# Performance work log

Measured on AMD Instinct MI355X. Metric: run time of the kernel, lower is better.

Reference implementation:

```python
import jax, jax.numpy as jnp
import numpy as np

N = 1024      # number of nodes
D = 128       # d_x
H = 8         # num_heads


def setup_inputs() -> dict:
    key = jax.random.key(0)
    ks = jax.random.split(key, 7)
    s = (D * H) ** -0.5
    return {
        "x": jax.random.normal(ks[0], (N, D), dtype=jnp.float32),
        "spatial_encoding": jax.random.normal(ks[1], (N, N), dtype=jnp.float32),
        "edge_encoding": jax.random.normal(ks[2], (N, N), dtype=jnp.float32),
        "Wq": jax.random.normal(ks[3], (D * H, D), dtype=jnp.float32) * s,
        "Wk": jax.random.normal(ks[4], (D * H, D), dtype=jnp.float32) * s,
        "Wv": jax.random.normal(ks[5], (D * H, D), dtype=jnp.float32) * s,
        "Wo": jax.random.normal(ks[6], (D, D * H), dtype=jnp.float32) * s,
    }


def reference(x, spatial_encoding, edge_encoding, Wq, Wk, Wv, Wo):
    n, d = x.shape
    h = Wq.shape[0] // d
    scale = d ** -0.5
    # Linear (no bias), then the module's peculiar view: [n, d*h] -> [d, n, h]
    q = (x @ Wq.T).reshape(d, n, h)            # [d, n, h]
    k = (x @ Wk.T).reshape(d, n, h)            # [d, n, h]
    v = (x @ Wv.T).reshape(d, n, h)            # [d, n, h]
    # a = q @ k^T over head dim: [d, n, n]
    a = jnp.einsum('dnh,dmh->dnm', q, k) * scale
    a = a + spatial_encoding + edge_encoding   # [n,n] biases broadcast over d
    a = jax.nn.softmax(a, axis=2)
    # dropout is identity at inference
    out = jnp.einsum('dnm,dmh->dnh', a, v)     # [d, n, h]
    out = out.reshape(n, h * d)                # row-major reshape, same as torch
    return out @ Wo.T                          # [n, d]
```

## Files before the change

kernel.cpp:

```cpp
#include <hip/hip_runtime.h>
#include <hip/hip_bf16.h>
#include <math.h>

#define N_NODES 1024
#define D_DIM   128
#define H_HEADS 8
#define DH      1024

typedef short  short8 __attribute__((ext_vector_type(8)));
typedef float  f32x16 __attribute__((ext_vector_type(16)));
typedef float  f32x4  __attribute__((ext_vector_type(4)));
typedef unsigned short us4 __attribute__((ext_vector_type(4)));

static __device__ __forceinline__ unsigned short f2bf(float x) {
    __hip_bfloat16 h = __float2bfloat16(x);
    return *reinterpret_cast<unsigned short*>(&h);
}
static __device__ __forceinline__ unsigned cvt_pk_bf16(float lo, float hi) {
    unsigned r;
    asm volatile("v_cvt_pk_bf16_f32 %0, %1, %2" : "=v"(r) : "v"(lo), "v"(hi));
    return r;
}
static __device__ __forceinline__ void permlane32_swap(unsigned &a, unsigned &b) {
    asm volatile("v_permlane32_swap_b32 %0, %1" : "+v"(a), "+v"(b));
}
static __device__ __forceinline__ float fast_exp2(float x) {
    float r;
    asm("v_exp_f32 %0, %1" : "=v"(r) : "v"(x));
    return r;
}

__global__ __launch_bounds__(256) void prep_kernel(const float* __restrict__ x,
                                                   const float* __restrict__ Wq,
                                                   const float* __restrict__ Wk,
                                                   const float* __restrict__ Wv,
                                                   const float* __restrict__ sp,
                                                   const float* __restrict__ ed,
                                                   unsigned short* __restrict__ Q,
                                                   unsigned short* __restrict__ K,
                                                   unsigned short* __restrict__ V,
                                                   float* __restrict__ Bq) {
    __shared__ float tile[32][33];
    const int bid = blockIdx.x;
    const int tid = threadIdx.x;

    if (bid < 768) {
        const int lane = tid & 63, wvi = tid >> 6;
        const int l31 = lane & 31, hi = lane >> 5;
        const int m   = bid >> 8;
        const int rem = bid & 255;
        const int rb0 = (rem & 7) * 128 + wvi * 32;
        const int col = (rem >> 3) * 32 + l31;
        const float* W        = (m == 0) ? Wq : (m == 1) ? Wk : Wv;
        unsigned short* Out   = (m == 0) ? Q  : (m == 1) ? K  : V;
        const float osc = (m == 0) ? 0.12751879523173864f : 1.0f;

        const float* xrow = x + (size_t)(rb0 + l31) * 128 + 8 * hi;
        const float* wrow = W + (size_t)col * 128 + 8 * hi;

        f32x16 acc = {};
        #pragma unroll
        for (int ks = 0; ks < 8; ++ks) {
            float4 xa = *reinterpret_cast<const float4*>(xrow + ks * 16);
            float4 xb = *reinterpret_cast<const float4*>(xrow + ks * 16 + 4);
            float4 wa = *reinterpret_cast<const float4*>(wrow + ks * 16);
            float4 wb = *reinterpret_cast<const float4*>(wrow + ks * 16 + 4);
            union { short8 s8; unsigned u[4]; } af, bf;
            af.u[0] = cvt_pk_bf16(xa.x, xa.y); af.u[1] = cvt_pk_bf16(xa.z, xa.w);
            af.u[2] = cvt_pk_bf16(xb.x, xb.y); af.u[3] = cvt_pk_bf16(xb.z, xb.w);
            bf.u[0] = cvt_pk_bf16(wa.x, wa.y); bf.u[1] = cvt_pk_bf16(wa.z, wa.w);
            bf.u[2] = cvt_pk_bf16(wb.x, wb.y); bf.u[3] = cvt_pk_bf16(wb.z, wb.w);
            acc = __builtin_amdgcn_mfma_f32_32x32x16_bf16(af.s8, bf.s8, acc, 0, 0, 0);
        }
        #pragma unroll
        for (int i = 0; i < 16; ++i) {
            int mm = (i & 3) + 8 * (i >> 2) + 4 * hi;
            Out[(size_t)(rb0 + mm) * DH + col] = f2bf(acc[i] * osc);
        }
    } else {
        const int b2 = bid - 768;
        const int cb = b2 & 31, rb = b2 >> 5;
        const float L2E = 1.4426950408889634f;
        for (int i = tid; i < 1024; i += 256) {
            int rr = i >> 5, cc = i & 31;
            size_t g = (size_t)(rb * 32 + rr) * 1024 + cb * 32 + cc;
            tile[rr][cc] = (sp[g] + ed[g]) * L2E;
        }
        __syncthreads();
        const int c4l = tid >> 5, rr = tid & 31;
        float4 v = make_float4(tile[rr][4 * c4l + 0], tile[rr][4 * c4l + 1],
                               tile[rr][4 * c4l + 2], tile[rr][4 * c4l + 3]);
        reinterpret_cast<float4*>(Bq)[(size_t)(cb * 8 + c4l) * 1024 + rb * 32 + rr] = v;
    }
}

__global__ __launch_bounds__(256) void attn_kernel(const unsigned short* __restrict__ Qb,
                                                   const unsigned short* __restrict__ Kb,
                                                   const unsigned short* __restrict__ Vb,
                                                   const float* __restrict__ Bq,
                                                   float* __restrict__ Opart,
                                                   float* __restrict__ Lpart) {
    __shared__ unsigned short Vt[9 * 512];
    const int dd = blockIdx.y, ch = blockIdx.z;
    const int tid = threadIdx.x, lane = tid & 63, wvi = tid >> 6;
    const int l31 = lane & 31, hi = lane >> 5;

    {
        const unsigned short* src = Vb + (size_t)dd * 8192 + (size_t)ch * 4096;
        char* base = reinterpret_cast<char*>(Vt);
        int pr = tid;
        short8 v0 = *reinterpret_cast<const short8*>(src + (size_t)(2 * pr) * 8);
        short8 v1 = *reinterpret_cast<const short8*>(src + (size_t)(2 * pr + 1) * 8);
        #pragma unroll
        for (int h = 0; h < 8; ++h) {
            unsigned d = (unsigned)(unsigned short)v0[h] |
                         ((unsigned)(unsigned short)v1[h] << 16);
            *reinterpret_cast<unsigned*>(base + h * 1024 + ((4 * pr) ^ (h << 4))) = d;
        }
        reinterpret_cast<unsigned*>(base + 8 * 1024)[tid] = 0x3F803F80u;
    }
    __syncthreads();

    const int r = blockIdx.x * 128 + wvi * 32 + l31;
    short8 qf = {};
    if (!hi) qf = *reinterpret_cast<const short8*>(Qb + (size_t)dd * 8192 + (size_t)r * 8);

    f32x16 oacc = {};
    const unsigned short* kp = Kb + (size_t)dd * 8192 + (size_t)(ch * 512 + l31) * 8;
    const float4* bq4 = reinterpret_cast<const float4*>(Bq)
                        + (size_t)ch * 131072 + (size_t)hi * 1024 + r;

    auto load_bias = [&](int cbv) -> f32x16 {
        const float4* b = bq4 + (size_t)cbv * 8192;
        float4 b0 = b[0], b1 = b[2048], b2 = b[4096], b3 = b[6144];
        f32x16 o;
        o[0] = b0.x; o[1] = b0.y; o[2]  = b0.z; o[3]  = b0.w;
        o[4] = b1.x; o[5] = b1.y; o[6]  = b1.z; o[7]  = b1.w;
        o[8] = b2.x; o[9] = b2.y; o[10] = b2.z; o[11] = b2.w;
        o[12] = b3.x; o[13] = b3.y; o[14] = b3.z; o[15] = b3.w;
        return o;
    };
    auto load_k = [&](int cbv) -> short8 {
        return *reinterpret_cast<const short8*>(kp + (size_t)cbv * 256);
    };
    auto step = [&](int cbv, const f32x16& bias, const short8& kfv) {
        f32x16 sf = bias;
        sf = __builtin_amdgcn_mfma_f32_32x32x16_bf16(kfv, qf, sf, 0, 0, 0);
        float p[16];
        #pragma unroll
        for (int i = 0; i < 16; ++i) p[i] = fast_exp2(sf[i]);
        unsigned u0 = cvt_pk_bf16(p[0],  p[1]);
        unsigned u1 = cvt_pk_bf16(p[2],  p[3]);
        unsigned u2 = cvt_pk_bf16(p[4],  p[5]);
        unsigned u3 = cvt_pk_bf16(p[6],  p[7]);
        unsigned u4 = cvt_pk_bf16(p[8],  p[9]);
        unsigned u5 = cvt_pk_bf16(p[10], p[11]);
        unsigned u6 = cvt_pk_bf16(p[12], p[13]);
        unsigned u7 = cvt_pk_bf16(p[14], p[15]);
        permlane32_swap(u0, u2);
        permlane32_swap(u1, u3);
        permlane32_swap(u4, u6);
        permlane32_swap(u5, u7);
        union { short8 s8; unsigned u[4]; } pb1, pb2;
        pb1.u[0] = u0; pb1.u[1] = u1; pb1.u[2] = u2; pb1.u[3] = u3;
        pb2.u[0] = u4; pb2.u[1] = u5; pb2.u[2] = u6; pb2.u[3] = u7;

        short8 vf1 = {}, vf2 = {};
        if (l31 < 9) {
            const char* vb = reinterpret_cast<const char*>(Vt) + l31 * 1024;
            vf1 = *reinterpret_cast<const short8*>(vb + ((cbv * 64 + 16 * hi)      ^ (l31 << 4)));
            vf2 = *reinterpret_cast<const short8*>(vb + ((cbv * 64 + 32 + 16 * hi) ^ (l31 << 4)));
        }
        oacc = __builtin_amdgcn_mfma_f32_32x32x16_bf16(vf1, pb1.s8, oacc, 0, 0, 0);
        oacc = __builtin_amdgcn_mfma_f32_32x32x16_bf16(vf2, pb2.s8, oacc, 0, 0, 0);
    };

    f32x16 bA = load_bias(0), bB = load_bias(1);
    short8 kA = load_k(0),   kB = load_k(1);
    for (int cb = 0; cb < 16; cb += 2) {
        step(cb, bA, kA);
        if (cb < 14) { bA = load_bias(cb + 2); kA = load_k(cb + 2); }
        step(cb + 1, bB, kB);
        if (cb < 14) { bB = load_bias(cb + 3); kB = load_k(cb + 3); }
    }

    size_t off = (size_t)ch * 1048576 + (size_t)dd * 8192 + (size_t)r * 8 + 4 * hi;
    *reinterpret_cast<float4*>(Opart + off) =
        make_float4(oacc[0], oacc[1], oacc[2], oacc[3]);
    if (!hi) Lpart[(size_t)ch * 131072 + (size_t)dd * 1024 + r] = oacc[4];
}

__global__ __launch_bounds__(256) void combine_kernel(const float* __restrict__ Opart,
                                                      const float* __restrict__ Lpart,
                                                      unsigned short* __restrict__ Oh,
                                                      unsigned short* __restrict__ Ol) {
    const int gid = blockIdx.x * 256 + threadIdx.x;
    const float4* p1 = reinterpret_cast<const float4*>(Opart) + (size_t)gid * 2;
    const float4* p2 = reinterpret_cast<const float4*>(Opart + 1048576) + (size_t)gid * 2;
    float4 a0 = p1[0], a1 = p1[1], b0 = p2[0], b1 = p2[1];
    const float rl = 1.f / (Lpart[gid] + Lpart[131072 + gid]);
    float v[8] = { (a0.x + b0.x) * rl, (a0.y + b0.y) * rl,
                   (a0.z + b0.z) * rl, (a0.w + b0.w) * rl,
                   (a1.x + b1.x) * rl, (a1.y + b1.y) * rl,
                   (a1.z + b1.z) * rl, (a1.w + b1.w) * rl };
    union { short8 s8; unsigned short us[8]; } h8, l8;
    #pragma unroll
    for (int i = 0; i < 8; ++i) {
        unsigned uv = __float_as_uint(v[i]);
        h8.us[i] = (unsigned short)(uv >> 16);
        l8.us[i] = f2bf(v[i] - __uint_as_float(uv & 0xFFFF0000u));
    }
    *reinterpret_cast<short8*>(Oh + (size_t)gid * 8) = h8.s8;
    *reinterpret_cast<short8*>(Ol + (size_t)gid * 8) = l8.s8;
}

__global__ __launch_bounds__(256) void oproj_kernel(const unsigned short* __restrict__ Oh,
                                                    const unsigned short* __restrict__ Ol,
                                                    const float* __restrict__ Wo,
                                                    float* __restrict__ out) {
    __shared__ float red[4][256];
    const int tid = threadIdx.x, lane = tid & 63, wvi = tid >> 6;
    const int l15 = lane & 15, kg = lane >> 4;
    const int rbase = blockIdx.x * 16, cbase = blockIdx.y * 16;

    const unsigned short* ah_p = Oh + (size_t)(rbase + l15) * 1024 + wvi * 256 + kg * 8;
    const unsigned short* al_p = Ol + (size_t)(rbase + l15) * 1024 + wvi * 256 + kg * 8;
    const float*          b_p  = Wo + (size_t)(cbase + l15) * 1024 + wvi * 256 + kg * 8;

    f32x4 acc = {};
    #pragma unroll
    for (int ks = 0; ks < 8; ++ks) {
        short8 ah = *reinterpret_cast<const short8*>(ah_p + ks * 32);
        short8 al = *reinterpret_cast<const short8*>(al_p + ks * 32);
        float4 w0 = *reinterpret_cast<const float4*>(b_p + ks * 32);
        float4 w1 = *reinterpret_cast<const float4*>(b_p + ks * 32 + 4);
        float w[8] = { w0.x, w0.y, w0.z, w0.w, w1.x, w1.y, w1.z, w1.w };
        union { short8 s8; unsigned u[4]; } bh, bl;
        #pragma unroll
        for (int j = 0; j < 4; ++j) {
            unsigned e = __float_as_uint(w[2 * j]) >> 16;
            unsigned o = __float_as_uint(w[2 * j + 1]) & 0xFFFF0000u;
            bh.u[j] = e | o;
            float lo0 = w[2 * j]     - __uint_as_float(__float_as_uint(w[2 * j])     & 0xFFFF0000u);
            float lo1 = w[2 * j + 1] - __uint_as_float(__float_as_uint(w[2 * j + 1]) & 0xFFFF0000u);
            bl.u[j] = cvt_pk_bf16(lo0, lo1);
        }
        acc = __builtin_amdgcn_mfma_f32_16x16x32_bf16(ah, bh.s8, acc, 0, 0, 0);
        acc = __builtin_amdgcn_mfma_f32_16x16x32_bf16(al, bh.s8, acc, 0, 0, 0);
        acc = __builtin_amdgcn_mfma_f32_16x16x32_bf16(ah, bl.s8, acc, 0, 0, 0);
    }
    #pragma unroll
    for (int i = 0; i < 4; ++i)
        red[wvi][(kg * 4 + i) * 16 + l15] = acc[i];
    __syncthreads();
    float v = red[0][tid & 255] + red[1][tid & 255] + red[2][tid & 255] + red[3][tid & 255];
    out[(size_t)(rbase + (tid >> 4)) * D_DIM + cbase + (tid & 15)] = v;
}

extern "C" void kernel_launch(void* const* d_in, const int* in_sizes, int n_in,
                              void* d_out, int out_size, void* d_ws, size_t ws_size,
                              hipStream_t stream) {
    const float* x  = (const float*)d_in[0];
    const float* sp = (const float*)d_in[1];
    const float* ed = (const float*)d_in[2];
    const float* Wq = (const float*)d_in[3];
    const float* Wk = (const float*)d_in[4];
    const float* Wv = (const float*)d_in[5];
    const float* Wo = (const float*)d_in[6];
    float* out = (float*)d_out;

    float* ws = (float*)d_ws;
    const size_t M = (size_t)N_NODES * DH;
    float* Bq = ws;
    unsigned short* Qb = (unsigned short*)(ws + M);
    unsigned short* Kb = Qb + M;
    unsigned short* Vb = Kb + M;
    unsigned short* Oh = Vb + M;
    unsigned short* Ol = Oh + M;
    float* Opart = (float*)(Ol + M);
    float* Lpart = Opart + 2 * M;

    prep_kernel<<<dim3(1792), 256, 0, stream>>>(x, Wq, Wk, Wv, sp, ed, Qb, Kb, Vb, Bq);
    attn_kernel<<<dim3(8, 128, 2), 256, 0, stream>>>(Qb, Kb, Vb, Bq, Opart, Lpart);
    combine_kernel<<<dim3(512), 256, 0, stream>>>(Opart, Lpart, Oh, Ol);
    oproj_kernel<<<dim3(64, 8), 256, 0, stream>>>(Oh, Ol, Wo, out);
}
```

Baseline: 66.42 us.

## Process two d-slices per attention block to reuse bias loads; pre-split Wo in prep

Each attention block now handles two d-slices, so the loaded bias tile (the dominant memory stream) is reused across both, and the grid shrinks by half in the y dimension. The V row index is clamped instead of predicated, which removes a branch. Separately, the bf16 hi/lo split of Wo moves into extra prep blocks written to workspace, so oproj loads pre-split bf16 instead of converting fp32 on the fly. The cost is higher register pressure (two accumulators, extra K and Q fragments) and fewer blocks in the attention launch.

```diff
diff --git a/kernel.cpp b/kernel.cpp
--- a/kernel.cpp
+++ b/kernel.cpp
@@ -10,7 +10,6 @@
 typedef short  short8 __attribute__((ext_vector_type(8)));
 typedef float  f32x16 __attribute__((ext_vector_type(16)));
 typedef float  f32x4  __attribute__((ext_vector_type(4)));
-typedef unsigned short us4 __attribute__((ext_vector_type(4)));
 
 static __device__ __forceinline__ unsigned short f2bf(float x) {
     __hip_bfloat16 h = __float2bfloat16(x);
@@ -36,10 +35,13 @@
                                                    const float* __restrict__ Wv,
                                                    const float* __restrict__ sp,
                                                    const float* __restrict__ ed,
+                                                   const float* __restrict__ Wo,
                                                    unsigned short* __restrict__ Q,
                                                    unsigned short* __restrict__ K,
                                                    unsigned short* __restrict__ V,
-                                                   float* __restrict__ Bq) {
+                                                   float* __restrict__ Bq,
+                                                   unsigned short* __restrict__ Woh,
+                                                   unsigned short* __restrict__ Wol) {
     __shared__ float tile[32][33];
     const int bid = blockIdx.x;
     const int tid = threadIdx.x;
@@ -77,7 +79,7 @@
             int mm = (i & 3) + 8 * (i >> 2) + 4 * hi;
             Out[(size_t)(rb0 + mm) * DH + col] = f2bf(acc[i] * osc);
         }
-    } else {
+    } else if (bid < 1792) {
         const int b2 = bid - 768;
         const int cb = b2 & 31, rb = b2 >> 5;
         const float L2E = 1.4426950408889634f;
@@ -91,6 +93,23 @@
         float4 v = make_float4(tile[rr][4 * c4l + 0], tile[rr][4 * c4l + 1],
                                tile[rr][4 * c4l + 2], tile[rr][4 * c4l + 3]);
         reinterpret_cast<float4*>(Bq)[(size_t)(cb * 8 + c4l) * 1024 + rb * 32 + rr] = v;
+    } else {
+        const int b2 = bid - 1792;
+        const size_t base = (size_t)b2 * 4096 + (size_t)tid * 16;
+        #pragma unroll
+        for (int t = 0; t < 4; ++t) {
+            float4 w = *reinterpret_cast<const float4*>(Wo + base + t * 4);
+            float ww[4] = { w.x, w.y, w.z, w.w };
+            unsigned short h4[4], l4[4];
+            #pragma unroll
+            for (int j = 0; j < 4; ++j) {
+                unsigned uv = __float_as_uint(ww[j]);
+                h4[j] = (unsigned short)(uv >> 16);
+                l4[j] = f2bf(ww[j] - __uint_as_float(uv & 0xFFFF0000u));
+            }
+            *reinterpret_cast<uint2*>(Woh + base + t * 4) = *reinterpret_cast<uint2*>(h4);
+            *reinterpret_cast<uint2*>(Wol + base + t * 4) = *reinterpret_cast<uint2*>(l4);
+        }
     }
 }
 
@@ -100,14 +119,15 @@
                                                    const float* __restrict__ Bq,
                                                    float* __restrict__ Opart,
                                                    float* __restrict__ Lpart) {
-    __shared__ unsigned short Vt[9 * 512];
-    const int dd = blockIdx.y, ch = blockIdx.z;
+    __shared__ unsigned short Vt[2][4608];
+    const int dp = blockIdx.y, ch = blockIdx.z;
     const int tid = threadIdx.x, lane = tid & 63, wvi = tid >> 6;
     const int l31 = lane & 31, hi = lane >> 5;
 
-    {
-        const unsigned short* src = Vb + (size_t)dd * 8192 + (size_t)ch * 4096;
-        char* base = reinterpret_cast<char*>(Vt);
+    #pragma unroll
+    for (int s = 0; s < 2; ++s) {
+        const unsigned short* src = Vb + (size_t)(2 * dp + s) * 8192 + (size_t)ch * 4096;
+        char* base = reinterpret_cast<char*>(&Vt[s][0]);
         int pr = tid;
         short8 v0 = *reinterpret_cast<const short8*>(src + (size_t)(2 * pr) * 8);
         short8 v1 = *reinterpret_cast<const short8*>(src + (size_t)(2 * pr + 1) * 8);
@@ -122,30 +142,36 @@
     __syncthreads();
 
     const int r = blockIdx.x * 128 + wvi * 32 + l31;
-    short8 qf = {};
-    if (!hi) qf = *reinterpret_cast<const short8*>(Qb + (size_t)dd * 8192 + (size_t)r * 8);
-
-    f32x16 oacc = {};
-    const unsigned short* kp = Kb + (size_t)dd * 8192 + (size_t)(ch * 512 + l31) * 8;
+    short8 qf0 = {}, qf1 = {};
+    if (!hi) {
+        qf0 = *reinterpret_cast<const short8*>(Qb + (size_t)(2 * dp)     * 8192 + (size_t)r * 8);
+        qf1 = *reinterpret_cast<const short8*>(Qb + (size_t)(2 * dp + 1) * 8192 + (size_t)r * 8);
+    }
+
+    f32x16 o0 = {}, o1 = {};
+    const unsigned short* kp0 = Kb + (size_t)(2 * dp) * 8192 + (size_t)(ch * 512 + l31) * 8;
+    const unsigned short* kp1 = kp0 + 8192;
     const float4* bq4 = reinterpret_cast<const float4*>(Bq)
                         + (size_t)ch * 131072 + (size_t)hi * 1024 + r;
+    const int vrow = (l31 < 8) ? l31 : 8;
+    const char* vb0 = reinterpret_cast<const char*>(&Vt[0][0]) + vrow * 1024;
+    const char* vb1 = reinterpret_cast<const char*>(&Vt[1][0]) + vrow * 1024;
+    const int vswz = vrow << 4;
 
     auto load_bias = [&](int cbv) -> f32x16 {
         const float4* b = bq4 + (size_t)cbv * 8192;
         float4 b0 = b[0], b1 = b[2048], b2 = b[4096], b3 = b[6144];
         f32x16 o;
-        o[0] = b0.x; o[1] = b0.y; o[2]  = b0.z; o[3]  = b0.w;
-        o[4] = b1.x; o[5] = b1.y; o[6]  = b1.z; o[7]  = b1.w;
-        o[8] = b2.x; o[9] = b2.y; o[10] = b2.z; o[11] = b2.w;
+        o[0]  = b0.x; o[1]  = b0.y; o[2]  = b0.z; o[3]  = b0.w;
+        o[4]  = b1.x; o[5]  = b1.y; o[6]  = b1.z; o[7]  = b1.w;
+        o[8]  = b2.x; o[9]  = b2.y; o[10] = b2.z; o[11] = b2.w;
         o[12] = b3.x; o[13] = b3.y; o[14] = b3.z; o[15] = b3.w;
         return o;
     };
-    auto load_k = [&](int cbv) -> short8 {
-        return *reinterpret_cast<const short8*>(kp + (size_t)cbv * 256);
-    };
-    auto step = [&](int cbv, const f32x16& bias, const short8& kfv) {
+    auto slice_step = [&](int cbv, const f32x16& bias, const short8& kfv,
+                          const short8& qfv, const char* vbs, f32x16& oaccs) {
         f32x16 sf = bias;
-        sf = __builtin_amdgcn_mfma_f32_32x32x16_bf16(kfv, qf, sf, 0, 0, 0);
+        sf = __builtin_amdgcn_mfma_f32_32x32x16_bf16(kfv, qfv, sf, 0, 0, 0);
         float p[16];
         #pragma unroll
         for (int i = 0; i < 16; ++i) p[i] = fast_exp2(sf[i]);
@@ -165,29 +191,36 @@
         pb1.u[0] = u0; pb1.u[1] = u1; pb1.u[2] = u2; pb1.u[3] = u3;
         pb2.u[0] = u4; pb2.u[1] = u5; pb2.u[2] = u6; pb2.u[3] = u7;
 
-        short8 vf1 = {}, vf2 = {};
-        if (l31 < 9) {
-            const char* vb = reinterpret_cast<const char*>(Vt) + l31 * 1024;
-            vf1 = *reinterpret_cast<const short8*>(vb + ((cbv * 64 + 16 * hi)      ^ (l31 << 4)));
-            vf2 = *reinterpret_cast<const short8*>(vb + ((cbv * 64 + 32 + 16 * hi) ^ (l31 << 4)));
-        }
-        oacc = __builtin_amdgcn_mfma_f32_32x32x16_bf16(vf1, pb1.s8, oacc, 0, 0, 0);
-        oacc = __builtin_amdgcn_mfma_f32_32x32x16_bf16(vf2, pb2.s8, oacc, 0, 0, 0);
+        short8 vf1 = *reinterpret_cast<const short8*>(vbs + ((cbv * 64 + 16 * hi)      ^ vswz));
+        short8 vf2 = *reinterpret_cast<const short8*>(vbs + ((cbv * 64 + 32 + 16 * hi) ^ vswz));
+        oaccs = __builtin_amdgcn_mfma_f32_32x32x16_bf16(vf1, pb1.s8, oaccs, 0, 0, 0);
+        oaccs = __builtin_amdgcn_mfma_f32_32x32x16_bf16(vf2, pb2.s8, oaccs, 0, 0, 0);
     };
+    auto load_k = [&](const unsigned short* kp, int cbv) -> short8 {
+        return *reinterpret_cast<const short8*>(kp + (size_t)cbv * 256);
+    };
 
     f32x16 bA = load_bias(0), bB = load_bias(1);
-    short8 kA = load_k(0),   kB = load_k(1);
+    short8 kA0 = load_k(kp0, 0), kA1 = load_k(kp1, 0);
+    short8 kB0 = load_k(kp0, 1), kB1 = load_k(kp1, 1);
     for (int cb = 0; cb < 16; cb += 2) {
-        step(cb, bA, kA);
-        if (cb < 14) { bA = load_bias(cb + 2); kA = load_k(cb + 2); }
-        step(cb + 1, bB, kB);
-        if (cb < 14) { bB = load_bias(cb + 3); kB = load_k(cb + 3); }
-    }
-
-    size_t off = (size_t)ch * 1048576 + (size_t)dd * 8192 + (size_t)r * 8 + 4 * hi;
-    *reinterpret_cast<float4*>(Opart + off) =
-        make_float4(oacc[0], oacc[1], oacc[2], oacc[3]);
-    if (!hi) Lpart[(size_t)ch * 131072 + (size_t)dd * 1024 + r] = oacc[4];
+        slice_step(cb, bA, kA0, qf0, vb0, o0);
+        slice_step(cb, bA, kA1, qf1, vb1, o1);
+        if (cb < 14) { bA = load_bias(cb + 2); kA0 = load_k(kp0, cb + 2); kA1 = load_k(kp1, cb + 2); }
+        slice_step(cb + 1, bB, kB0, qf0, vb0, o0);
+        slice_step(cb + 1, bB, kB1, qf1, vb1, o1);
+        if (cb < 14) { bB = load_bias(cb + 3); kB0 = load_k(kp0, cb + 3); kB1 = load_k(kp1, cb + 3); }
+    }
+
+    #pragma unroll
+    for (int s = 0; s < 2; ++s) {
+        const f32x16& oa = s ? o1 : o0;
+        const int dd = 2 * dp + s;
+        size_t off = (size_t)ch * 1048576 + (size_t)dd * 8192 + (size_t)r * 8 + 4 * hi;
+        *reinterpret_cast<float4*>(Opart + off) =
+            make_float4(oa[0], oa[1], oa[2], oa[3]);
+        if (!hi) Lpart[(size_t)ch * 131072 + (size_t)dd * 1024 + r] = oa[4];
+    }
 }
 
 __global__ __launch_bounds__(256) void combine_kernel(const float* __restrict__ Opart,
@@ -216,38 +249,29 @@
 
 __global__ __launch_bounds__(256) void oproj_kernel(const unsigned short* __restrict__ Oh,
                                                     const unsigned short* __restrict__ Ol,
-                                                    const float* __restrict__ Wo,
+                                                    const unsigned short* __restrict__ Woh,
+                                                    const unsigned short* __restrict__ Wol,
                                                     float* __restrict__ out) {
     __shared__ float red[4][256];
     const int tid = threadIdx.x, lane = tid & 63, wvi = tid >> 6;
     const int l15 = lane & 15, kg = lane >> 4;
     const int rbase = blockIdx.x * 16, cbase = blockIdx.y * 16;
 
-    const unsigned short* ah_p = Oh + (size_t)(rbase + l15) * 1024 + wvi * 256 + kg * 8;
-    const unsigned short* al_p = Ol + (size_t)(rbase + l15) * 1024 + wvi * 256 + kg * 8;
-    const float*          b_p  = Wo + (size_t)(cbase + l15) * 1024 + wvi * 256 + kg * 8;
+    const unsigned short* ah_p = Oh  + (size_t)(rbase + l15) * 1024 + wvi * 256 + kg * 8;
+    const unsigned short* al_p = Ol  + (size_t)(rbase + l15) * 1024 + wvi * 256 + kg * 8;
+    const unsigned short* bh_p = Woh + (size_t)(cbase + l15) * 1024 + wvi * 256 + kg * 8;
+    const unsigned short* bl_p = Wol + (size_t)(cbase + l15) * 1024 + wvi * 256 + kg * 8;
 
     f32x4 acc = {};
     #pragma unroll
     for (int ks = 0; ks < 8; ++ks) {
         short8 ah = *reinterpret_cast<const short8*>(ah_p + ks * 32);
         short8 al = *reinterpret_cast<const short8*>(al_p + ks * 32);
-        float4 w0 = *reinterpret_cast<const float4*>(b_p + ks * 32);
-        float4 w1 = *reinterpret_cast<const float4*>(b_p + ks * 32 + 4);
-        float w[8] = { w0.x, w0.y, w0.z, w0.w, w1.x, w1.y, w1.z, w1.w };
-        union { short8 s8; unsigned u[4]; } bh, bl;
-        #pragma unroll
-        for (int j = 0; j < 4; ++j) {
-            unsigned e = __float_as_uint(w[2 * j]) >> 16;
-            unsigned o = __float_as_uint(w[2 * j + 1]) & 0xFFFF0000u;
-            bh.u[j] = e | o;
-            float lo0 = w[2 * j]     - __uint_as_float(__float_as_uint(w[2 * j])     & 0xFFFF0000u);
-            float lo1 = w[2 * j + 1] - __uint_as_float(__float_as_uint(w[2 * j + 1]) & 0xFFFF0000u);
-            bl.u[j] = cvt_pk_bf16(lo0, lo1);
-        }
-        acc = __builtin_amdgcn_mfma_f32_16x16x32_bf16(ah, bh.s8, acc, 0, 0, 0);
-        acc = __builtin_amdgcn_mfma_f32_16x16x32_bf16(al, bh.s8, acc, 0, 0, 0);
-        acc = __builtin_amdgcn_mfma_f32_16x16x32_bf16(ah, bl.s8, acc, 0, 0, 0);
+        short8 bh = *reinterpret_cast<const short8*>(bh_p + ks * 32);
+        short8 bl = *reinterpret_cast<const short8*>(bl_p + ks * 32);
+        acc = __builtin_amdgcn_mfma_f32_16x16x32_bf16(ah, bh, acc, 0, 0, 0);
+        acc = __builtin_amdgcn_mfma_f32_16x16x32_bf16(al, bh, acc, 0, 0, 0);
+        acc = __builtin_amdgcn_mfma_f32_16x16x32_bf16(ah, bl, acc, 0, 0, 0);
     }
     #pragma unroll
     for (int i = 0; i < 4; ++i)
@@ -279,9 +303,12 @@
     unsigned short* Ol = Oh + M;
     float* Opart = (float*)(Ol + M);
     float* Lpart = Opart + 2 * M;
-
-    prep_kernel<<<dim3(1792), 256, 0, stream>>>(x, Wq, Wk, Wv, sp, ed, Qb, Kb, Vb, Bq);
-    attn_kernel<<<dim3(8, 128, 2), 256, 0, stream>>>(Qb, Kb, Vb, Bq, Opart, Lpart);
+    unsigned short* Woh = (unsigned short*)(Lpart + 2 * 131072);
+    unsigned short* Wol = Woh + 131072;
+
+    prep_kernel<<<dim3(1824), 256, 0, stream>>>(x, Wq, Wk, Wv, sp, ed, Wo,
+                                                Qb, Kb, Vb, Bq, Woh, Wol);
+    attn_kernel<<<dim3(8, 64, 2), 256, 0, stream>>>(Qb, Kb, Vb, Bq, Opart, Lpart);
     combine_kernel<<<dim3(512), 256, 0, stream>>>(Opart, Lpart, Oh, Ol);
-    oproj_kernel<<<dim3(64, 8), 256, 0, stream>>>(Oh, Ol, Wo, out);
-}
+    oproj_kernel<<<dim3(64, 8), 256, 0, stream>>>(Oh, Ol, Woh, Wol, out);
+}
```

New measurement: 62.97 us. 1.05x faster.
